# Kernel optimization log

Measured on AMD Instinct MI355X. Metric: run time of the kernel, lower is better.

Reference implementation:

```python
import jax, jax.numpy as jnp
import numpy as np

NUM_QUERIES = 150
NEG = 1e9


def setup_inputs() -> dict:
    key = jax.random.key(0)
    ks = jax.random.split(key, 5)
    B, C, H, W = 4, 256, 64, 64
    img_feat = jax.random.normal(ks[0], (B, C, H, W), dtype=jnp.float32)
    exe_feat = jax.random.normal(ks[1], (B, C), dtype=jnp.float32)
    mask = jax.random.bernoulli(ks[2], 0.9, (B, H, W)).astype(jnp.float32)
    # similarity initialized as identity (plus tiny noise so it's non-degenerate)
    similarity = jnp.eye(C, dtype=jnp.float32) + 0.01 * jax.random.normal(ks[3], (C, C), dtype=jnp.float32)
    # nn.Linear weight, shape (out, in)
    v_w = jax.random.normal(ks[4], (C, C), dtype=jnp.float32) / np.sqrt(C)
    return {"img_feat": img_feat, "exe_feat": exe_feat, "mask": mask,
            "similarity": similarity, "v_w": v_w}


def _get_queries(attn, B, H, W):
    # peak detection on similarity-to-exemplar channel (last column), no grad
    simil = jax.lax.stop_gradient(attn[:, :, -1]).reshape(B, H, W)
    c = simil[:, 1:-1, 1:-1]
    is_max = ((c > simil[:, :-2, 1:-1]) &   # strictly greater than above
              (c >= simil[:, 2:, 1:-1]) &   # >= below
              (c > simil[:, 1:-1, :-2]) &   # strictly greater than left
              (c >= simil[:, 1:-1, 2:]))    # >= right
    pen = jnp.zeros_like(simil).at[:, 1:-1, 1:-1].set(
        jnp.where(is_max, 0.0, NEG))
    scores = (simil - pen).reshape(B, H * W)
    _, q_ids = jax.lax.top_k(scores, NUM_QUERIES)  # [B, Q]
    return q_ids


def reference(img_feat, exe_feat, mask, similarity, v_w):
    B, C, H, W = img_feat.shape
    HW = H * W
    unrolled = img_feat.reshape(B, C, HW)                      # [B,C,HW]
    exe = (exe_feat * 1.2)[:, :, None]                         # [B,C,1]
    concat = jnp.concatenate([unrolled, exe], axis=2)          # [B,C,HW+1]
    # values = Linear(concat^T): x @ W^T
    values = jnp.einsum('bcn,dc->bnd', concat, v_w)            # [B,HW+1,C]
    # attn = unrolled^T @ similarity @ concat
    attn = jnp.einsum('bcn,cd,bdm->bnm', unrolled, similarity, concat)  # [B,HW,HW+1]

    q_ids = _get_queries(attn, B, H, W)                        # [B,Q] int
    queries = jnp.take_along_axis(values[:, :-1], q_ids[:, :, None], axis=1)  # [B,Q,C]

    # masked softmax: outer product of pixel mask, exemplar column always kept
    m = jax.lax.stop_gradient(mask).reshape(B, HW)
    mm = m[:, :, None] * m[:, None, :]                         # [B,HW,HW]
    mm = jnp.concatenate([mm, jnp.ones((B, HW, 1), mm.dtype)], axis=2)
    attn = attn - (mm != 1).astype(attn.dtype) * NEG
    attn = jax.nn.softmax(attn, axis=2)

    new_img = jnp.einsum('bnm,bmd->bnd', attn, values)         # [B,HW,C]
    new_img = new_img.transpose(0, 2, 1).reshape(B, C, H, W)
    return new_img + img_feat, queries
```

## Files before the change

### kernel.cpp

```cpp
#include <hip/hip_runtime.h>

#define CC   256
#define HWS  4096
#define MPAD 4160
#define NB   4
#define NTIL 65

typedef __attribute__((ext_vector_type(8))) short   short8;
typedef __attribute__((ext_vector_type(4))) float   floatx4;

static __device__ __forceinline__ short8 ld8(const unsigned short* p) {
  return *(const short8*)p;
}
static __device__ __forceinline__ void st8(unsigned short* p, short8 v) {
  *(short8*)p = v;
}
static __device__ __forceinline__ unsigned short f2b(float x) {
  union { float f; unsigned u; } v; v.f = x;
  unsigned r = v.u + 0x7FFFu + ((v.u >> 16) & 1u);
  return (unsigned short)(r >> 16);
}
static __device__ __forceinline__ float b2f(unsigned short x) {
  union { unsigned u; float f; } v; v.u = ((unsigned)x) << 16;
  return v.f;
}

__global__ void prep_mats(const float* __restrict__ sim, const float* __restrict__ vw,
                          unsigned short* __restrict__ St, unsigned short* __restrict__ Vw) {
  int dd = blockIdx.x, c = threadIdx.x;
  St[dd*CC + c] = f2b(sim[c*CC + dd]);
  Vw[dd*CC + c] = f2b(vw[dd*CC + c]);
}

__global__ void colb_kernel(const float* __restrict__ mask, float* __restrict__ colb) {
  int b = blockIdx.x, tid = threadIdx.x;
  for (int m = tid; m < MPAD; m += 256) {
    float v;
    if (m < HWS)      v = (mask[b*HWS + m] - 1.0f) * 1e9f;
    else if (m == HWS) v = 0.0f;
    else               v = -3.0e38f;
    colb[b*MPAD + m] = v;
  }
}

__global__ void build_kt(const float* __restrict__ img, const float* __restrict__ exe,
                         unsigned short* __restrict__ Kt) {
  int b = blockIdx.x, mt = blockIdx.y, dt = blockIdx.z;
  int tid = threadIdx.x;
  int m0 = mt*64, d0 = dt*64;
  if (mt == 64) {
    for (int i = 0; i < 16; ++i) {
      int m = m0 + (tid>>6) + i*4;
      int d = d0 + (tid&63);
      unsigned short v = 0;
      if (m == 4096) v = f2b(1.2f * exe[b*CC + d]);
      Kt[((size_t)b*MPAD + m)*CC + d] = v;
    }
    return;
  }
  __shared__ float tile[64][65];
  for (int i = 0; i < 16; ++i) {
    int dl = (tid>>6) + i*4, ml = tid&63;
    tile[dl][ml] = img[((size_t)b*CC + d0+dl)*HWS + m0+ml];
  }
  __syncthreads();
  for (int i = 0; i < 16; ++i) {
    int ml = (tid>>6) + i*4, dl = tid&63;
    Kt[((size_t)b*MPAD + m0+ml)*CC + d0+dl] = f2b(tile[dl][ml]);
  }
}

__global__ __launch_bounds__(256) void gemm_small(const unsigned short* __restrict__ Kt,
    const unsigned short* __restrict__ Bm, unsigned short* __restrict__ Tout,
    unsigned short* __restrict__ Vbt, int mode) {
  int b  = blockIdx.x;
  int r0 = blockIdx.y*64 + (threadIdx.x>>6)*16;
  int c0 = blockIdx.z*64;
  int lane = threadIdx.x & 63;
  int lo = lane & 15, hi = lane >> 4;
  floatx4 acc[4] = {};
  const unsigned short* arow = Kt + ((size_t)b*MPAD + r0 + lo)*CC + hi*8;
#pragma unroll
  for (int k = 0; k < 8; ++k) {
    short8 af = ld8(arow + k*32);
#pragma unroll
    for (int t = 0; t < 4; ++t) {
      short8 bf = ld8(Bm + (size_t)(c0 + t*16 + lo)*CC + k*32 + hi*8);
      acc[t] = __builtin_amdgcn_mfma_f32_16x16x32_bf16(af, bf, acc[t], 0, 0, 0);
    }
  }
  if (mode == 0) {
#pragma unroll
    for (int t = 0; t < 4; ++t)
#pragma unroll
      for (int r = 0; r < 4; ++r) {
        int n = r0 + hi*4 + r, dd = c0 + t*16 + lo;
        Tout[((size_t)b*HWS + n)*CC + dd] = f2b(acc[t][r]);
      }
  } else {
#pragma unroll
    for (int t = 0; t < 4; ++t)
#pragma unroll
      for (int r = 0; r < 4; ++r) {
        int m = r0 + hi*4 + r, dd = c0 + t*16 + lo;
        Vbt[((size_t)b*CC + dd)*MPAD + m] = f2b(acc[t][r]);
      }
  }
}

__global__ __launch_bounds__(256) void reorder_kv(const unsigned short* __restrict__ Kt,
    const unsigned short* __restrict__ Vbt, unsigned short* __restrict__ Kf,
    unsigned short* __restrict__ Vf) {
  int b = blockIdx.x, mt = blockIdx.y;
  int m0 = mt*64;
  int tid = threadIdx.x;
  int w = tid >> 6, lane = tid & 63;
  int lo = lane & 15, hi = lane >> 4;
  size_t tile = (size_t)(b*NTIL + mt)*16384;
  unsigned short* kf = Kf + tile;
  unsigned short* vf = Vf + tile;
  const unsigned short* ktb = Kt  + (size_t)b*MPAD*CC;
  const unsigned short* vtb = Vbt + (size_t)b*CC*MPAD;
#pragma unroll
  for (int i = 0; i < 8; ++i) {
    int s = i*4 + w;
    {
      int k = s >> 2, t = s & 3;
      short8 v = ld8(ktb + (size_t)(m0 + t*16 + lo)*CC + k*32 + hi*8);
      st8(kf + s*512 + lane*8, v);
    }
    {
      int h = s >> 4, t = s & 15;
      short8 v = ld8(vtb + (size_t)(t*16 + lo)*MPAD + m0 + h*32 + hi*8);
      st8(vf + s*512 + lane*8, v);
    }
  }
}

__global__ __launch_bounds__(256) void scores_kernel(const float* __restrict__ img,
    const float* __restrict__ sim, const float* __restrict__ exe,
    float* __restrict__ score32) {
  int b = blockIdx.x, n0 = blockIdx.y*16;
  int d = threadIdx.x;
  __shared__ float U[16][257];
  __shared__ float R[16][256];
  __shared__ float E[256];
  for (int idx = threadIdx.x; idx < 16*256; idx += 256) {
    int nl = idx & 15, c = idx >> 4;
    U[nl][c] = img[((size_t)b*CC + c)*HWS + n0 + nl];
  }
  E[d] = 1.2f * exe[b*CC + d];
  __syncthreads();
  float acc[16];
#pragma unroll
  for (int nl = 0; nl < 16; ++nl) acc[nl] = 0.f;
  for (int c = 0; c < CC; ++c) {
    float s_cd = sim[c*CC + d];
#pragma unroll
    for (int nl = 0; nl < 16; ++nl) acc[nl] = fmaf(U[nl][c], s_cd, acc[nl]);
  }
#pragma unroll
  for (int nl = 0; nl < 16; ++nl) R[nl][d] = acc[nl];
  __syncthreads();
  if (d < 16) {
    float s = 0.f;
    for (int dd = 0; dd < CC; ++dd) s = fmaf(R[d][dd], E[dd], s);
    score32[b*HWS + n0 + d] = s;
  }
}

__global__ __launch_bounds__(64) void select_kernel(const float* __restrict__ scores,
                                                    int* __restrict__ qids) {
  int b = blockIdx.x, lane = threadIdx.x;
  __shared__ float sc[HWS];
  __shared__ unsigned long long kx[HWS];
  __shared__ unsigned long long list[256];
  __shared__ unsigned int hist[256];
  __shared__ unsigned int st[4];
  __shared__ unsigned long long sh_base;

  const floatx4* s4 = (const floatx4*)(scores + (size_t)b*HWS);
  floatx4* c4 = (floatx4*)sc;
#pragma unroll
  for (int i = 0; i < 16; ++i) c4[i*64 + lane] = s4[i*64 + lane];
  __syncthreads();

  for (int i = 0; i < 64; ++i) {
    int idx = i*64 + lane;
    int y = i, x = lane;
    float c0 = sc[idx];
    float v = c0;
    if (y >= 1 && y <= 62 && x >= 1 && x <= 62) {
      bool ismax = (c0 > sc[idx-64]) && (c0 >= sc[idx+64]) &&
                   (c0 > sc[idx-1])  && (c0 >= sc[idx+1]);
      if (!ismax) v = c0 - 1e9f;
    }
    unsigned u = __float_as_uint(v);
    u = (u & 0x80000000u) ? ~u : (u | 0x80000000u);
    kx[idx] = (((unsigned long long)u) << 12) | (unsigned long long)(4095 - idx);
  }
  __syncthreads();

  unsigned long long base = 0;
  unsigned int need = 150, C = 0;
  for (int s = 36; s >= 4; s -= 8) {
    for (int i = lane; i < 256; i += 64) hist[i] = 0;
    __syncthreads();
    unsigned long long pref = base >> (s + 8);
    for (int i = 0; i < 64; ++i) {
      unsigned long long k = kx[i*64 + lane];
      if ((k >> (s + 8)) == pref) atomicAdd(&hist[(unsigned)(k >> s) & 255u], 1u);
    }
    __syncthreads();
    if (lane == 0) {
      unsigned cum = 0; int B = 0;
      for (int bin = 255; bin >= 0; --bin) {
        cum += hist[bin];
        if (cum >= need) { B = bin; break; }
      }
      st[0] = (150u - need) + cum;
      st[1] = need - (cum - hist[B]);
      sh_base = base | ((unsigned long long)B << s);
    }
    __syncthreads();
    C = st[0]; need = st[1]; base = sh_base;
    if (C <= 256u) break;
  }

  if (lane == 0) st[2] = 0;
  __syncthreads();
  for (int i = 0; i < 64; ++i) {
    unsigned long long k = kx[i*64 + lane];
    if (k >= base) {
      unsigned p = atomicAdd(&st[2], 1u);
      list[p] = k;
    }
  }
  __syncthreads();
  for (int i = lane; i < 256; i += 64) if (i >= (int)C) list[i] = 0ull;
  __syncthreads();

  for (int kk = 2; kk <= 256; kk <<= 1) {
    for (int j = kk >> 1; j > 0; j >>= 1) {
#pragma unroll
      for (int tt = 0; tt < 2; ++tt) {
        int t = lane + tt*64;
        int i2 = ((t & ~(j - 1)) << 1) | (t & (j - 1));
        int p2 = i2 | j;
        bool desc = ((i2 & kk) == 0);
        unsigned long long a = list[i2], c = list[p2];
        bool sw = desc ? (a < c) : (a > c);
        if (sw) { list[i2] = c; list[p2] = a; }
      }
      __syncthreads();
    }
  }

  for (int q = lane; q < 150; q += 64)
    qids[b*150 + q] = 4095 - (int)(list[q] & 0xFFFull);
}

__global__ __launch_bounds__(256, 1) void flash_kernel(
    const unsigned short* __restrict__ Tb, const unsigned short* __restrict__ Kt,
    const unsigned short* __restrict__ Kf, const unsigned short* __restrict__ Vf,
    const float* __restrict__ mask, const float* __restrict__ colb,
    const float* __restrict__ img, float* __restrict__ out0) {
  int blk = blockIdx.x;
  int b   = (blk & 7) >> 1;
  int g   = ((blk >> 3) << 1) | (blk & 1);
  int bn0 = g << 6;
  int tid = threadIdx.x;
  int wave = tid >> 6, lane = tid & 63;
  int lo = lane & 15, hi = lane >> 4;
  int n0 = bn0 + wave*16;

  __shared__ unsigned short pbuf[4][1152];
  unsigned short* plw = &pbuf[wave][0];

  short8 q[8];
  const unsigned short* tb = Tb + ((size_t)b*HWS + n0 + lo)*CC + hi*8;
#pragma unroll
  for (int k = 0; k < 8; ++k) q[k] = ld8(tb + k*32);

  const float* mk = mask + b*HWS;

  float ddot = 0.f, edot = 0.f;
  {
    const unsigned short* kdp = Kt + ((size_t)b*MPAD + n0 + lo)*CC + hi*8;
    const unsigned short* kep = Kt + ((size_t)b*MPAD + HWS)*CC + hi*8;
#pragma unroll
    for (int k = 0; k < 8; ++k) {
      short8 kd = ld8(kdp + k*32);
      short8 ke = ld8(kep + k*32);
#pragma unroll
      for (int j = 0; j < 8; ++j) {
        float qf = b2f((unsigned short)q[k][j]);
        ddot = fmaf(qf, b2f((unsigned short)kd[j]), ddot);
        edot = fmaf(qf, b2f((unsigned short)ke[j]), edot);
      }
    }
    ddot += __shfl_xor(ddot, 16); ddot += __shfl_xor(ddot, 32);
    edot += __shfl_xor(edot, 16); edot += __shfl_xor(edot, 32);
  }
  float Mrow = ((mk[n0 + lo] == 1.0f) ? ddot : edot) + 2.0f;
  float* fM = (float*)plw;
  fM[lo] = Mrow;
  float crb[4], Msub[4];
#pragma unroll
  for (int r = 0; r < 4; ++r) {
    Msub[r] = fM[hi*4 + r];
    crb[r]  = (mk[n0 + hi*4 + r] - 1.0f)*1e9f - Msub[r];
  }

  float lsum[4] = {0.f, 0.f, 0.f, 0.f};
  floatx4 o[16] = {};

  const unsigned short* kfb = Kf + (size_t)b*NTIL*16384 + lane*8;
  const unsigned short* vfb = Vf + (size_t)b*NTIL*16384 + lane*8;
  const float* cbb = colb + b*MPAD;

  short8 ka[32], va[32];
#pragma unroll
  for (int s2 = 0; s2 < 32; ++s2) ka[s2] = ld8(kfb + s2*512);

  for (int mt = 0; mt < NTIL; ++mt) {
    int m0 = mt*64;
    const unsigned short* vs = vfb + (size_t)mt*16384;
#pragma unroll
    for (int s2 = 0; s2 < 32; ++s2) va[s2] = ld8(vs + s2*512);
    floatx4 s[4] = {};
#pragma unroll
    for (int k = 0; k < 8; ++k)
#pragma unroll
      for (int t = 0; t < 4; ++t)
        s[t] = __builtin_amdgcn_mfma_f32_16x16x32_bf16(q[k], ka[k*4 + t], s[t], 0, 0, 0);
    if (mt + 1 < NTIL) {
      const unsigned short* ks = kfb + (size_t)(mt+1)*16384;
#pragma unroll
      for (int s2 = 0; s2 < 32; ++s2) ka[s2] = ld8(ks + s2*512);
    }
    float cb[4];
#pragma unroll
    for (int t = 0; t < 4; ++t) cb[t] = cbb[m0 + t*16 + lo];
    float pr[4][4];
#pragma unroll
    for (int t = 0; t < 4; ++t)
#pragma unroll
      for (int r = 0; r < 4; ++r)
        pr[t][r] = s[t][r] + cb[t] + crb[r];
    if (mt == NTIL-1 && lo == 0) {
#pragma unroll
      for (int r = 0; r < 4; ++r) pr[0][r] = s[0][r] - Msub[r];
    }
#pragma unroll
    for (int t = 0; t < 4; ++t)
#pragma unroll
      for (int r = 0; r < 4; ++r) {
        float p = __expf(pr[t][r]);
        lsum[r] += p;
        plw[(hi*4 + r)*72 + t*16 + lo] = f2b(p);
      }
    short8 pf0 = *(const short8*)&plw[lo*72 + hi*8];
    short8 pf1 = *(const short8*)&plw[lo*72 + 32 + hi*8];
#pragma unroll
    for (int sl = 0; sl < 32; ++sl)
      o[sl & 15] = __builtin_amdgcn_mfma_f32_16x16x32_bf16((sl >> 4) ? pf1 : pf0,
                                                           va[sl], o[sl & 15], 0, 0, 0);
  }
#pragma unroll
  for (int r = 0; r < 4; ++r) {
#pragma unroll
    for (int off = 1; off < 16; off <<= 1) lsum[r] += __shfl_xor(lsum[r], off);
  }
  float inv[4];
#pragma unroll
  for (int r = 0; r < 4; ++r) inv[r] = 1.0f / lsum[r];
  const float* ib = img  + (size_t)b*CC*HWS;
  float*       ob = out0 + (size_t)b*CC*HWS;
#pragma unroll
  for (int c = 0; c < 4; ++c) {
#pragma unroll
    for (int tp = 0; tp < 4; ++tp) {
      int t = c*4 + tp;
#pragma unroll
      for (int r = 0; r < 4; ++r)
        plw[(hi*4 + r)*66 + tp*16 + lo] = f2b(o[t][r]*inv[r]);
    }
#pragma unroll
    for (int j = 0; j < 16; ++j) {
      int d = c*64 + hi*16 + j;
      float v = b2f(plw[lo*66 + hi*16 + j]);
      size_t idx = (size_t)d*HWS + n0 + lo;
      ob[idx] = v + ib[idx];
    }
  }
}

__global__ __launch_bounds__(256) void gather_kernel(const float* __restrict__ img,
    const float* __restrict__ vw, const int* __restrict__ qids, float* __restrict__ out1) {
  int blk = blockIdx.x;
  int b = blk / 150, q = blk % 150;
  int dd = threadIdx.x;
  __shared__ float col[CC];
  int id = qids[b*150 + q];
  col[dd] = img[((size_t)b*CC + dd)*HWS + id];
  __syncthreads();
  const float* vr = vw + dd*CC;
  float acc = 0.f;
  for (int c = 0; c < CC; ++c) acc = fmaf(col[c], vr[c], acc);
  out1[((size_t)(b*150 + q))*CC + dd] = acc;
}

extern "C" void kernel_launch(void* const* d_in, const int* in_sizes, int n_in,
                              void* d_out, int out_size, void* d_ws, size_t ws_size,
                              hipStream_t stream) {
  const float* img  = (const float*)d_in[0];
  const float* exe  = (const float*)d_in[1];
  const float* mask = (const float*)d_in[2];
  const float* sim  = (const float*)d_in[3];
  const float* vw   = (const float*)d_in[4];
  float* out0 = (float*)d_out;
  float* out1 = out0 + (size_t)NB*CC*HWS;

  char* ws = (char*)d_ws;
  size_t o = 0;
  unsigned short* Kt  = (unsigned short*)(ws + o); o += (size_t)NB*MPAD*CC*2;
  unsigned short* Tb  = (unsigned short*)(ws + o); o += (size_t)NB*HWS*CC*2;
  unsigned short* Vbt = (unsigned short*)(ws + o); o += (size_t)NB*CC*MPAD*2;
  unsigned short* Kf  = (unsigned short*)(ws + o); o += (size_t)NB*NTIL*16384*2;
  unsigned short* Vf  = (unsigned short*)(ws + o); o += (size_t)NB*NTIL*16384*2;
  unsigned short* St  = (unsigned short*)(ws + o); o += (size_t)CC*CC*2;
  unsigned short* Vw  = (unsigned short*)(ws + o); o += (size_t)CC*CC*2;
  float*          scores = (float*)(ws + o);       o += (size_t)NB*HWS*4;
  float*          colb   = (float*)(ws + o);       o += (size_t)NB*MPAD*4;
  int*            qids   = (int*)(ws + o);         o += (size_t)NB*150*4;

  prep_mats  <<<dim3(CC),         dim3(CC),  0, stream>>>(sim, vw, St, Vw);
  colb_kernel<<<dim3(NB),         dim3(256), 0, stream>>>(mask, colb);
  build_kt   <<<dim3(NB, 65, 4),  dim3(256), 0, stream>>>(img, exe, Kt);
  gemm_small <<<dim3(NB, 64, 4),  dim3(256), 0, stream>>>(Kt, St, Tb, nullptr, 0);
  gemm_small <<<dim3(NB, 65, 4),  dim3(256), 0, stream>>>(Kt, Vw, nullptr, Vbt, 1);
  reorder_kv <<<dim3(NB, NTIL),   dim3(256), 0, stream>>>(Kt, Vbt, Kf, Vf);
  scores_kernel<<<dim3(NB, 256),  dim3(256), 0, stream>>>(img, sim, exe, scores);
  select_kernel<<<dim3(NB),       dim3(64),  0, stream>>>(scores, qids);
  flash_kernel <<<dim3(256),      dim3(256), 0, stream>>>(Tb, Kt, Kf, Vf, mask, colb, img, out0);
  gather_kernel<<<dim3(NB*150),   dim3(256), 0, stream>>>(img, vw, qids, out1);
}
```

Measured before the change: 402.9 us.

## Stage K/V tiles in LDS via async global_load_lds with double buffering

The flash kernel now runs two waves per block, each handling 32 query rows instead of 16. K and V tiles are double-buffered in shared memory using direct global-to-LDS loads, replacing per-wave register loads of the whole tile. Each K/V fragment read from LDS now feeds two MFMAs, which halves the global K/V traffic per query row. The cost is higher register pressure from two accumulator sets, about 130KB of LDS, fewer waves per CU, and a block barrier on every tile.

```diff
diff --git a/kernel.cpp b/kernel.cpp
--- a/kernel.cpp
+++ b/kernel.cpp
@@ -23,6 +23,11 @@
 static __device__ __forceinline__ float b2f(unsigned short x) {
   union { unsigned u; float f; } v; v.u = ((unsigned)x) << 16;
   return v.f;
+}
+static __device__ __forceinline__ void gl_lds16(const unsigned short* g, unsigned short* l) {
+  __builtin_amdgcn_global_load_lds(
+      (const __attribute__((address_space(1))) unsigned int*)g,
+      (__attribute__((address_space(3))) unsigned int*)l, 16, 0, 0);
 }
 
 __global__ void prep_mats(const float* __restrict__ sim, const float* __restrict__ vw,
@@ -260,7 +265,7 @@
     qids[b*150 + q] = 4095 - (int)(list[q] & 0xFFFull);
 }
 
-__global__ __launch_bounds__(256, 1) void flash_kernel(
+__global__ __launch_bounds__(128, 1) void flash_kernel(
     const unsigned short* __restrict__ Tb, const unsigned short* __restrict__ Kt,
     const unsigned short* __restrict__ Kf, const unsigned short* __restrict__ Vf,
     const float* __restrict__ mask, const float* __restrict__ colb,
@@ -272,109 +277,182 @@
   int tid = threadIdx.x;
   int wave = tid >> 6, lane = tid & 63;
   int lo = lane & 15, hi = lane >> 4;
-  int n0 = bn0 + wave*16;
-
-  __shared__ unsigned short pbuf[4][1152];
+  int n0 = bn0 + wave*32;
+
+  __shared__ unsigned short kvK[2][16384];
+  __shared__ unsigned short kvV[2][16384];
+  __shared__ unsigned short pbuf[2][1152];
   unsigned short* plw = &pbuf[wave][0];
 
-  short8 q[8];
-  const unsigned short* tb = Tb + ((size_t)b*HWS + n0 + lo)*CC + hi*8;
-#pragma unroll
-  for (int k = 0; k < 8; ++k) q[k] = ld8(tb + k*32);
+  const unsigned short* kfb = Kf + (size_t)b*NTIL*16384;
+  const unsigned short* vfb = Vf + (size_t)b*NTIL*16384;
+
+#pragma unroll
+  for (int i = 0; i < 16; ++i) {
+    int s = wave*16 + i;
+    gl_lds16(kfb + s*512 + lane*8, &kvK[0][s*512]);
+    gl_lds16(vfb + s*512 + lane*8, &kvV[0][s*512]);
+  }
+
+  short8 q0[8], q1[8];
+  const unsigned short* tb0 = Tb + ((size_t)b*HWS + n0 + lo)*CC + hi*8;
+#pragma unroll
+  for (int k = 0; k < 8; ++k) { q0[k] = ld8(tb0 + k*32); q1[k] = ld8(tb0 + 16*CC + k*32); }
 
   const float* mk = mask + b*HWS;
 
-  float ddot = 0.f, edot = 0.f;
+  float crb0[4], Msub0[4], crb1[4], Msub1[4];
   {
+    const unsigned short* kep = Kt + ((size_t)b*MPAD + HWS)*CC + hi*8;
+    float ddot = 0.f, edot = 0.f;
     const unsigned short* kdp = Kt + ((size_t)b*MPAD + n0 + lo)*CC + hi*8;
-    const unsigned short* kep = Kt + ((size_t)b*MPAD + HWS)*CC + hi*8;
 #pragma unroll
     for (int k = 0; k < 8; ++k) {
       short8 kd = ld8(kdp + k*32);
       short8 ke = ld8(kep + k*32);
 #pragma unroll
       for (int j = 0; j < 8; ++j) {
-        float qf = b2f((unsigned short)q[k][j]);
+        float qf = b2f((unsigned short)q0[k][j]);
         ddot = fmaf(qf, b2f((unsigned short)kd[j]), ddot);
         edot = fmaf(qf, b2f((unsigned short)ke[j]), edot);
       }
     }
     ddot += __shfl_xor(ddot, 16); ddot += __shfl_xor(ddot, 32);
     edot += __shfl_xor(edot, 16); edot += __shfl_xor(edot, 32);
-  }
-  float Mrow = ((mk[n0 + lo] == 1.0f) ? ddot : edot) + 2.0f;
-  float* fM = (float*)plw;
-  fM[lo] = Mrow;
-  float crb[4], Msub[4];
-#pragma unroll
-  for (int r = 0; r < 4; ++r) {
-    Msub[r] = fM[hi*4 + r];
-    crb[r]  = (mk[n0 + hi*4 + r] - 1.0f)*1e9f - Msub[r];
-  }
-
-  float lsum[4] = {0.f, 0.f, 0.f, 0.f};
-  floatx4 o[16] = {};
-
-  const unsigned short* kfb = Kf + (size_t)b*NTIL*16384 + lane*8;
-  const unsigned short* vfb = Vf + (size_t)b*NTIL*16384 + lane*8;
+    float Mrow = ((mk[n0 + lo] == 1.0f) ? ddot : edot) + 2.0f;
+    float* fM = (float*)plw;
+    fM[lo] = Mrow;
+#pragma unroll
+    for (int r = 0; r < 4; ++r) {
+      Msub0[r] = fM[hi*4 + r];
+      crb0[r]  = (mk[n0 + hi*4 + r] - 1.0f)*1e9f - Msub0[r];
+    }
+    ddot = 0.f; edot = 0.f;
+    const unsigned short* kdp1 = Kt + ((size_t)b*MPAD + n0 + 16 + lo)*CC + hi*8;
+#pragma unroll
+    for (int k = 0; k < 8; ++k) {
+      short8 kd = ld8(kdp1 + k*32);
+      short8 ke = ld8(kep + k*32);
+#pragma unroll
+      for (int j = 0; j < 8; ++j) {
+        float qf = b2f((unsigned short)q1[k][j]);
+        ddot = fmaf(qf, b2f((unsigned short)kd[j]), ddot);
+        edot = fmaf(qf, b2f((unsigned short)ke[j]), edot);
+      }
+    }
+    ddot += __shfl_xor(ddot, 16); ddot += __shfl_xor(ddot, 32);
+    edot += __shfl_xor(edot, 16); edot += __shfl_xor(edot, 32);
+    float Mrow1 = ((mk[n0 + 16 + lo] == 1.0f) ? ddot : edot) + 2.0f;
+    fM[lo] = Mrow1;
+#pragma unroll
+    for (int r = 0; r < 4; ++r) {
+      Msub1[r] = fM[hi*4 + r];
+      crb1[r]  = (mk[n0 + 16 + hi*4 + r] - 1.0f)*1e9f - Msub1[r];
+    }
+  }
+
+  float lsum0[4] = {0.f, 0.f, 0.f, 0.f};
+  float lsum1[4] = {0.f, 0.f, 0.f, 0.f};
+  floatx4 o0[16] = {};
+  floatx4 o1[16] = {};
   const float* cbb = colb + b*MPAD;
 
-  short8 ka[32], va[32];
-#pragma unroll
-  for (int s2 = 0; s2 < 32; ++s2) ka[s2] = ld8(kfb + s2*512);
+  __syncthreads();
 
   for (int mt = 0; mt < NTIL; ++mt) {
-    int m0 = mt*64;
-    const unsigned short* vs = vfb + (size_t)mt*16384;
-#pragma unroll
-    for (int s2 = 0; s2 < 32; ++s2) va[s2] = ld8(vs + s2*512);
-    floatx4 s[4] = {};
-#pragma unroll
-    for (int k = 0; k < 8; ++k)
-#pragma unroll
-      for (int t = 0; t < 4; ++t)
-        s[t] = __builtin_amdgcn_mfma_f32_16x16x32_bf16(q[k], ka[k*4 + t], s[t], 0, 0, 0);
+    int cur = mt & 1;
     if (mt + 1 < NTIL) {
       const unsigned short* ks = kfb + (size_t)(mt+1)*16384;
-#pragma unroll
-      for (int s2 = 0; s2 < 32; ++s2) ka[s2] = ld8(ks + s2*512);
-    }
+      const unsigned short* vs = vfb + (size_t)(mt+1)*16384;
+#pragma unroll
+      for (int i = 0; i < 16; ++i) {
+        int s = wave*16 + i;
+        gl_lds16(ks + s*512 + lane*8, &kvK[cur^1][s*512]);
+        gl_lds16(vs + s*512 + lane*8, &kvV[cur^1][s*512]);
+      }
+    }
+    int m0 = mt*64;
+    const unsigned short* kb = &kvK[cur][lane*8];
+    const unsigned short* vb = &kvV[cur][lane*8];
+    floatx4 s0[4] = {}, s1[4] = {};
+#pragma unroll
+    for (int k = 0; k < 8; ++k)
+#pragma unroll
+      for (int t = 0; t < 4; ++t) {
+        short8 kf = ld8(kb + (k*4 + t)*512);
+        s0[t] = __builtin_amdgcn_mfma_f32_16x16x32_bf16(q0[k], kf, s0[t], 0, 0, 0);
+        s1[t] = __builtin_amdgcn_mfma_f32_16x16x32_bf16(q1[k], kf, s1[t], 0, 0, 0);
+      }
     float cb[4];
 #pragma unroll
     for (int t = 0; t < 4; ++t) cb[t] = cbb[m0 + t*16 + lo];
-    float pr[4][4];
-#pragma unroll
-    for (int t = 0; t < 4; ++t)
-#pragma unroll
-      for (int r = 0; r < 4; ++r)
-        pr[t][r] = s[t][r] + cb[t] + crb[r];
-    if (mt == NTIL-1 && lo == 0) {
-#pragma unroll
-      for (int r = 0; r < 4; ++r) pr[0][r] = s[0][r] - Msub[r];
-    }
-#pragma unroll
-    for (int t = 0; t < 4; ++t)
-#pragma unroll
-      for (int r = 0; r < 4; ++r) {
-        float p = __expf(pr[t][r]);
-        lsum[r] += p;
-        plw[(hi*4 + r)*72 + t*16 + lo] = f2b(p);
-      }
-    short8 pf0 = *(const short8*)&plw[lo*72 + hi*8];
-    short8 pf1 = *(const short8*)&plw[lo*72 + 32 + hi*8];
-#pragma unroll
-    for (int sl = 0; sl < 32; ++sl)
-      o[sl & 15] = __builtin_amdgcn_mfma_f32_16x16x32_bf16((sl >> 4) ? pf1 : pf0,
-                                                           va[sl], o[sl & 15], 0, 0, 0);
-  }
+    short8 pf00, pf01, pf10, pf11;
+    {
+      float pr[4][4];
+#pragma unroll
+      for (int t = 0; t < 4; ++t)
+#pragma unroll
+        for (int r = 0; r < 4; ++r)
+          pr[t][r] = s0[t][r] + cb[t] + crb0[r];
+      if (mt == NTIL-1 && lo == 0) {
+#pragma unroll
+        for (int r = 0; r < 4; ++r) pr[0][r] = s0[0][r] - Msub0[r];
+      }
+#pragma unroll
+      for (int t = 0; t < 4; ++t)
+#pragma unroll
+        for (int r = 0; r < 4; ++r) {
+          float p = __expf(pr[t][r]);
+          lsum0[r] += p;
+          plw[(hi*4 + r)*72 + t*16 + lo] = f2b(p);
+        }
+      pf00 = *(const short8*)&plw[lo*72 + hi*8];
+      pf01 = *(const short8*)&plw[lo*72 + 32 + hi*8];
+    }
+    {
+      float pr[4][4];
+#pragma unroll
+      for (int t = 0; t < 4; ++t)
+#pragma unroll
+        for (int r = 0; r < 4; ++r)
+          pr[t][r] = s1[t][r] + cb[t] + crb1[r];
+      if (mt == NTIL-1 && lo == 0) {
+#pragma unroll
+        for (int r = 0; r < 4; ++r) pr[0][r] = s1[0][r] - Msub1[r];
+      }
+#pragma unroll
+      for (int t = 0; t < 4; ++t)
+#pragma unroll
+        for (int r = 0; r < 4; ++r) {
+          float p = __expf(pr[t][r]);
+          lsum1[r] += p;
+          plw[(hi*4 + r)*72 + t*16 + lo] = f2b(p);
+        }
+      pf10 = *(const short8*)&plw[lo*72 + hi*8];
+      pf11 = *(const short8*)&plw[lo*72 + 32 + hi*8];
+    }
+#pragma unroll
+    for (int sl = 0; sl < 32; ++sl) {
+      short8 vf = ld8(vb + sl*512);
+      o0[sl & 15] = __builtin_amdgcn_mfma_f32_16x16x32_bf16((sl >> 4) ? pf01 : pf00,
+                                                            vf, o0[sl & 15], 0, 0, 0);
+      o1[sl & 15] = __builtin_amdgcn_mfma_f32_16x16x32_bf16((sl >> 4) ? pf11 : pf10,
+                                                            vf, o1[sl & 15], 0, 0, 0);
+    }
+    __syncthreads();
+  }
+
 #pragma unroll
   for (int r = 0; r < 4; ++r) {
 #pragma unroll
-    for (int off = 1; off < 16; off <<= 1) lsum[r] += __shfl_xor(lsum[r], off);
-  }
-  float inv[4];
-#pragma unroll
-  for (int r = 0; r < 4; ++r) inv[r] = 1.0f / lsum[r];
+    for (int off = 1; off < 16; off <<= 1) {
+      lsum0[r] += __shfl_xor(lsum0[r], off);
+      lsum1[r] += __shfl_xor(lsum1[r], off);
+    }
+  }
+  float inv0[4], inv1[4];
+#pragma unroll
+  for (int r = 0; r < 4; ++r) { inv0[r] = 1.0f / lsum0[r]; inv1[r] = 1.0f / lsum1[r]; }
   const float* ib = img  + (size_t)b*CC*HWS;
   float*       ob = out0 + (size_t)b*CC*HWS;
 #pragma unroll
@@ -384,13 +462,30 @@
       int t = c*4 + tp;
 #pragma unroll
       for (int r = 0; r < 4; ++r)
-        plw[(hi*4 + r)*66 + tp*16 + lo] = f2b(o[t][r]*inv[r]);
+        plw[(hi*4 + r)*66 + tp*16 + lo] = f2b(o0[t][r]*inv0[r]);
     }
 #pragma unroll
     for (int j = 0; j < 16; ++j) {
       int d = c*64 + hi*16 + j;
       float v = b2f(plw[lo*66 + hi*16 + j]);
       size_t idx = (size_t)d*HWS + n0 + lo;
+      ob[idx] = v + ib[idx];
+    }
+  }
+#pragma unroll
+  for (int c = 0; c < 4; ++c) {
+#pragma unroll
+    for (int tp = 0; tp < 4; ++tp) {
+      int t = c*4 + tp;
+#pragma unroll
+      for (int r = 0; r < 4; ++r)
+        plw[(hi*4 + r)*66 + tp*16 + lo] = f2b(o1[t][r]*inv1[r]);
+    }
+#pragma unroll
+    for (int j = 0; j < 16; ++j) {
+      int d = c*64 + hi*16 + j;
+      float v = b2f(plw[lo*66 + hi*16 + j]);
+      size_t idx = (size_t)d*HWS + n0 + 16 + lo;
       ob[idx] = v + ib[idx];
     }
   }
@@ -443,6 +538,6 @@
   reorder_kv <<<dim3(NB, NTIL),   dim3(256), 0, stream>>>(Kt, Vbt, Kf, Vf);
   scores_kernel<<<dim3(NB, 256),  dim3(256), 0, stream>>>(img, sim, exe, scores);
   select_kernel<<<dim3(NB),       dim3(64),  0, stream>>>(scores, qids);
-  flash_kernel <<<dim3(256),      dim3(256), 0, stream>>>(Tb, Kt, Kf, Vf, mask, colb, img, out0);
+  flash_kernel <<<dim3(256),      dim3(128), 0, stream>>>(Tb, Kt, Kf, Vf, mask, colb, img, out0);
   gather_kernel<<<dim3(NB*150),   dim3(256), 0, stream>>>(img, vw, qids, out1);
 }
```

Measured after the change: 521.5 us. 29.4% more time.

## Stage K/V tiles cooperatively in double-buffered LDS via global_load_lds

Applied to the files above, without the earlier changes.

Previously each of the four waves loaded the full 64-column K and V tiles from global memory into its own registers, so every tile was fetched four times per block. Now the waves split each tile's load using direct global-to-LDS loads into double-buffered shared arrays, prefetching the next tile while the current one is consumed. The MFMA operands are read from LDS instead. This cuts redundant global/L2 traffic and register pressure, at the cost of roughly 128KB of LDS, extra LDS reads, and a block barrier per tile.

```diff
diff --git a/kernel.cpp b/kernel.cpp
--- a/kernel.cpp
+++ b/kernel.cpp
@@ -23,6 +23,11 @@
 static __device__ __forceinline__ float b2f(unsigned short x) {
   union { unsigned u; float f; } v; v.u = ((unsigned)x) << 16;
   return v.f;
+}
+static __device__ __forceinline__ void gl_lds16(const unsigned short* g, unsigned short* l) {
+  __builtin_amdgcn_global_load_lds(
+      (const __attribute__((address_space(1))) unsigned int*)g,
+      (__attribute__((address_space(3))) unsigned int*)l, 16, 0, 0);
 }
 
 __global__ void prep_mats(const float* __restrict__ sim, const float* __restrict__ vw,
@@ -274,8 +279,20 @@
   int lo = lane & 15, hi = lane >> 4;
   int n0 = bn0 + wave*16;
 
+  __shared__ unsigned short kvK[2][16384];
+  __shared__ unsigned short kvV[2][16384];
   __shared__ unsigned short pbuf[4][1152];
   unsigned short* plw = &pbuf[wave][0];
+
+  const unsigned short* kfb = Kf + (size_t)b*NTIL*16384;
+  const unsigned short* vfb = Vf + (size_t)b*NTIL*16384;
+
+#pragma unroll
+  for (int i = 0; i < 8; ++i) {
+    int s = wave*8 + i;
+    gl_lds16(kfb + s*512 + lane*8, &kvK[0][s*512]);
+    gl_lds16(vfb + s*512 + lane*8, &kvV[0][s*512]);
+  }
 
   short8 q[8];
   const unsigned short* tb = Tb + ((size_t)b*HWS + n0 + lo)*CC + hi*8;
@@ -314,31 +331,31 @@
 
   float lsum[4] = {0.f, 0.f, 0.f, 0.f};
   floatx4 o[16] = {};
-
-  const unsigned short* kfb = Kf + (size_t)b*NTIL*16384 + lane*8;
-  const unsigned short* vfb = Vf + (size_t)b*NTIL*16384 + lane*8;
   const float* cbb = colb + b*MPAD;
 
-  short8 ka[32], va[32];
-#pragma unroll
-  for (int s2 = 0; s2 < 32; ++s2) ka[s2] = ld8(kfb + s2*512);
+  __syncthreads();
 
   for (int mt = 0; mt < NTIL; ++mt) {
-    int m0 = mt*64;
-    const unsigned short* vs = vfb + (size_t)mt*16384;
-#pragma unroll
-    for (int s2 = 0; s2 < 32; ++s2) va[s2] = ld8(vs + s2*512);
-    floatx4 s[4] = {};
-#pragma unroll
-    for (int k = 0; k < 8; ++k)
-#pragma unroll
-      for (int t = 0; t < 4; ++t)
-        s[t] = __builtin_amdgcn_mfma_f32_16x16x32_bf16(q[k], ka[k*4 + t], s[t], 0, 0, 0);
+    int cur = mt & 1;
     if (mt + 1 < NTIL) {
       const unsigned short* ks = kfb + (size_t)(mt+1)*16384;
-#pragma unroll
-      for (int s2 = 0; s2 < 32; ++s2) ka[s2] = ld8(ks + s2*512);
-    }
+      const unsigned short* vs = vfb + (size_t)(mt+1)*16384;
+#pragma unroll
+      for (int i = 0; i < 8; ++i) {
+        int s = wave*8 + i;
+        gl_lds16(ks + s*512 + lane*8, &kvK[cur^1][s*512]);
+        gl_lds16(vs + s*512 + lane*8, &kvV[cur^1][s*512]);
+      }
+    }
+    int m0 = mt*64;
+    floatx4 s[4] = {};
+#pragma unroll
+    for (int k = 0; k < 8; ++k)
+#pragma unroll
+      for (int t = 0; t < 4; ++t) {
+        short8 kf = ld8(&kvK[cur][(k*4 + t)*512 + lane*8]);
+        s[t] = __builtin_amdgcn_mfma_f32_16x16x32_bf16(q[k], kf, s[t], 0, 0, 0);
+      }
     float cb[4];
 #pragma unroll
     for (int t = 0; t < 4; ++t) cb[t] = cbb[m0 + t*16 + lo];
@@ -363,9 +380,12 @@
     short8 pf0 = *(const short8*)&plw[lo*72 + hi*8];
     short8 pf1 = *(const short8*)&plw[lo*72 + 32 + hi*8];
 #pragma unroll
-    for (int sl = 0; sl < 32; ++sl)
+    for (int sl = 0; sl < 32; ++sl) {
+      short8 vfr = ld8(&kvV[cur][sl*512 + lane*8]);
       o[sl & 15] = __builtin_amdgcn_mfma_f32_16x16x32_bf16((sl >> 4) ? pf1 : pf0,
-                                                           va[sl], o[sl & 15], 0, 0, 0);
+                                                           vfr, o[sl & 15], 0, 0, 0);
+    }
+    __syncthreads();
   }
 #pragma unroll
   for (int r = 0; r < 4; ++r) {
```

Result: slower. 447.3 us (+11.0%).
